# Kernel tuning notes

Measured on AMD Instinct MI355X. Metric: run time of the kernel, lower is better.

Reference implementation:

```python
import jax, jax.numpy as jnp
import numpy as np

H = 128
GATE_CODES = (2, 3, 4, 1)  # order in original forward: NOT, AND, OR, MAJ


def gru_step(x, h, Wih, bih, Whh, bhh):
    # single-step PyTorch GRU math; weights stored transposed [H, 3H]
    gi = x @ Wih + bih
    gh = h @ Whh + bhh
    ir, iz, inn = jnp.split(gi, 3, axis=-1)
    hr, hz, hn = jnp.split(gh, 3, axis=-1)
    r = jax.nn.sigmoid(ir + hr)
    z = jax.nn.sigmoid(iz + hz)
    n = jnp.tanh(inn + r * hn)
    return (1.0 - z) * n + z * h


def setup_inputs() -> dict:
    key = jax.random.key(0)
    N, E, L = 60000, 180000, 3
    ks = jax.random.split(key, 16)

    def p(k, shape, fan_in):
        return (jax.random.normal(k, shape, jnp.float32) / np.float32(np.sqrt(fan_in)))

    return dict(
        gate=jax.random.randint(ks[0], (N,), 0, 6),
        edge_index=jax.random.randint(ks[1], (2, E), 0, N),
        forward_level=jax.random.randint(ks[2], (N,), 0, L),
        num_levels=L,
        Ws_self=p(ks[3], (6, H), 6), Ws_nbr=p(ks[4], (6, H), 6),
        Wt_self=p(ks[5], (6, H), 6), Wt_nbr=p(ks[6], (6, H), 6),
        hs_W=p(ks[7], (2 * H, H), 2 * H), hs_b=jnp.zeros((H,), jnp.float32),
        aggr_W1=p(ks[8], (4, 2 * H, H), 2 * H), aggr_b1=jnp.zeros((4, H), jnp.float32),
        aggr_W2=p(ks[9], (4, H, H), H), aggr_b2=jnp.zeros((4, H), jnp.float32),
        gru_Wih=p(ks[10], (4, H, 3 * H), H), gru_bih=jnp.zeros((4, 3 * H), jnp.float32),
        gru_Whh=p(ks[11], (4, H, 3 * H), H), gru_bhh=jnp.zeros((4, 3 * H), jnp.float32),
    )


def reference(gate, edge_index, forward_level, num_levels,
              Ws_self, Ws_nbr, Wt_self, Wt_nbr, hs_W, hs_b,
              aggr_W1, aggr_b1, aggr_W2, aggr_b2,
              gru_Wih, gru_bih, gru_Whh, gru_bhh):
    N = gate.shape[0]
    src, dst = edge_index[0], edge_index[1]

    # struct encoder: one-hop MP producing source/target embeddings s, t [N, H]
    one_hot = jax.nn.one_hot(gate, 6, dtype=jnp.float32)
    nbr_in = jax.ops.segment_sum(one_hot[src], dst, num_segments=N)
    nbr_out = jax.ops.segment_sum(one_hot[dst], src, num_segments=N)
    s = jax.nn.relu(one_hot @ Ws_self + nbr_in @ Ws_nbr)
    t = jax.nn.relu(one_hot @ Wt_self + nbr_out @ Wt_nbr)

    hs = jnp.concatenate([s, t], -1) @ hs_W + hs_b          # [N, H]
    hf = jnp.zeros((N, H), jnp.float32)

    gate_dst = gate[dst]
    lvl_dst = forward_level[dst]
    # num_rounds = 1; levels 1..num_levels-1, gate types disjoint per node
    for level in range(1, num_levels):
        node_state = jnp.concatenate([hs, hf], -1)           # [N, 2H]
        src_state = node_state[src]                          # [E, 2H] gather
        for gi, code in enumerate(GATE_CODES):
            emask = ((gate_dst == code) & (lvl_dst == level)).astype(jnp.float32)[:, None]
            msg = jax.nn.relu(src_state @ aggr_W1[gi] + aggr_b1[gi]) @ aggr_W2[gi] + aggr_b2[gi]
            agg = jax.ops.segment_sum(msg * emask, dst, num_segments=N)  # scatter-add
            h_new = gru_step(agg, hf, gru_Wih[gi], gru_bih[gi], gru_Whh[gi], gru_bhh[gi])
            nmask = ((gate == code) & (forward_level == level))[:, None]
            hf = jnp.where(nmask, h_new, hf)
    return hs, hf
```

## Files before the change

### kernel.cpp

```cpp
#include <hip/hip_runtime.h>
#include <limits.h>

#define H 128

typedef __bf16 bf16x8 __attribute__((ext_vector_type(8)));
typedef __bf16 bf16x4 __attribute__((ext_vector_type(4)));
typedef float  f32x4  __attribute__((ext_vector_type(4)));

#define CUR_SENTINEL (INT_MIN / 2)

__device__ __forceinline__ int gate_to_gi(int g) {
    switch (g) {
        case 2: return 0;
        case 3: return 1;
        case 4: return 2;
        case 1: return 3;
        default: return -1;
    }
}

__global__ __launch_bounds__(256)
void prep_weights(const float* __restrict__ aW1, const float* __restrict__ aW2,
                  const float* __restrict__ gWih, const float* __restrict__ hsW,
                  __bf16* __restrict__ W1T, __bf16* __restrict__ W2T,
                  __bf16* __restrict__ WihT, __bf16* __restrict__ hsWT,
                  f32x4* __restrict__ zbase, int zn16) {
    const int z = blockIdx.z;
    const int tid = threadIdx.x;
    if (z == 14) {
        f32x4 zero = {};
        for (int i = blockIdx.x * 256 + tid; i < zn16; i += gridDim.x * 256) zbase[i] = zero;
        return;
    }
    const float* src;
    __bf16* dst;
    int K, C;
    if (z < 4)       { src = aW1 + (size_t)z * 256 * 128;       dst = W1T + (size_t)z * 128 * 256; K = 256; C = 128; }
    else if (z < 8)  { src = aW2 + (size_t)(z - 4) * 128 * 128; dst = W2T + (size_t)(z - 4) * 128 * 128; K = 128; C = 128; }
    else if (z < 12) { src = gWih + (size_t)(z - 8) * 128 * 384; dst = WihT + (size_t)(z - 8) * 384 * 128; K = 128; C = 384; }
    else             { src = hsW;                                dst = hsWT;                        K = 256; C = 128; }
    __shared__ float tile[32][33];
    const int tilesC = C >> 5;
    const int ntile = (K >> 5) * tilesC;
    const int t = blockIdx.x;
    if (t >= ntile) return;
    const int k0 = (t / tilesC) << 5;
    const int c0 = (t % tilesC) << 5;
    #pragma unroll
    for (int e = 0; e < 4; ++e) {
        int pos = e * 256 + tid;
        int kk = pos >> 5, cc = pos & 31;
        tile[kk][cc] = src[(size_t)(k0 + kk) * C + c0 + cc];
    }
    __syncthreads();
    #pragma unroll
    for (int e = 0; e < 4; ++e) {
        int pos = e * 256 + tid;
        int cc = pos >> 5, kk = pos & 31;
        dst[(size_t)(c0 + cc) * K + k0 + kk] = (__bf16)tile[kk][cc];
    }
}

__global__ __launch_bounds__(256)
void hist_kernel(const int* __restrict__ gate, const int* __restrict__ ei, int E,
                 int* __restrict__ cnt_in, int* __restrict__ cnt_out) {
    int e = blockIdx.x * blockDim.x + threadIdx.x;
    if (e >= E) return;
    int s = ei[e], d = ei[E + e];
    atomicAdd(&cnt_in[d * 6 + gate[s]], 1);
    atomicAdd(&cnt_out[s * 6 + gate[d]], 1);
}

__global__ __launch_bounds__(256)
void node_alloc(const int* __restrict__ gate, const int* __restrict__ lvl,
                const int* __restrict__ cnt_in, int N, int ecap, int ncap,
                int* __restrict__ galloc, int* __restrict__ ncnt,
                int* __restrict__ cursor, int* __restrict__ nbuf) {
    __shared__ int lcnt[16];
    __shared__ int lbase[16];
    const int tid = threadIdx.x;
    for (int base = blockIdx.x * 256; base < N; base += gridDim.x * 256) {
        if (tid < 16) lcnt[tid] = 0;
        __syncthreads();
        int n = base + tid;
        int b = -1, local = 0, nlocal = 0;
        if (n < N) {
            int gi = gate_to_gi(gate[n]);
            int L = lvl[n];
            if (gi >= 0 && L >= 1 && L <= 2) {
                b = (L - 1) * 4 + gi;
                int deg = 0;
                #pragma unroll
                for (int c = 0; c < 6; ++c) deg += cnt_in[n * 6 + c];
                local = atomicAdd(&lcnt[b], deg);
                nlocal = atomicAdd(&lcnt[8 + b], 1);
            }
        }
        __syncthreads();
        if (tid < 8)       lbase[tid] = atomicAdd(&galloc[tid], lcnt[tid]);
        else if (tid < 16) lbase[tid] = atomicAdd(&ncnt[tid - 8], lcnt[tid]);
        __syncthreads();
        if (n < N) {
            if (b >= 0) {
                cursor[n] = b * ecap + lbase[b] + local;
                int p = lbase[8 + b] + nlocal;
                if (p < ncap) nbuf[b * ncap + p] = n;
            } else {
                cursor[n] = CUR_SENTINEL;
            }
        }
        __syncthreads();
    }
}

__global__ __launch_bounds__(256)
void edge_scatter(const int* __restrict__ ei, int E,
                  int* __restrict__ cursor, int2* __restrict__ elist) {
    int e = blockIdx.x * blockDim.x + threadIdx.x;
    if (e >= E) return;
    int d = ei[E + e];
    int slot = atomicAdd(&cursor[d], 1);
    if (slot >= 0) elist[slot] = make_int2(ei[e], d);
}

__global__ __launch_bounds__(256, 2)
void encoder_mfma(const int* __restrict__ gate, const int* __restrict__ lvl,
                  const int* __restrict__ cnt_in, const int* __restrict__ cnt_out,
                  const float* __restrict__ Ws_self, const float* __restrict__ Ws_nbr,
                  const float* __restrict__ Wt_self, const float* __restrict__ Wt_nbr,
                  const __bf16* __restrict__ hsWT, const float* __restrict__ hs_b,
                  float* __restrict__ out, __bf16* __restrict__ mir,
                  float* __restrict__ agg, int N) {
    __shared__ __bf16 st[16][264];
    const int tid = threadIdx.x;
    const int lane = tid & 63;
    const int w = tid >> 6;
    const int row = tid >> 4;
    const int c0 = (tid & 15) * 8;

    bf16x8 bw[8][2];
    #pragma unroll
    for (int kk = 0; kk < 8; ++kk)
        #pragma unroll
        for (int j = 0; j < 2; ++j) {
            int col = w * 32 + j * 16 + (lane & 15);
            bw[kk][j] = *(const bf16x8*)&hsWT[(size_t)col * 256 + kk * 32 + (lane >> 4) * 8];
        }
    float hbc[2];
    #pragma unroll
    for (int j = 0; j < 2; ++j) hbc[j] = hs_b[w * 32 + j * 16 + (lane & 15)];

    const int ntiles = (N + 15) >> 4;
    for (int t = blockIdx.x; t < ntiles; t += gridDim.x) {
        const int base = t * 16;
        int n = base + row;
        if (n >= N) n = N - 1;
        const int g = gate[n];
        const int L = lvl[n];
        int cin[6], cout[6];
        #pragma unroll
        for (int k = 0; k < 6; ++k) { cin[k] = cnt_in[n * 6 + k]; cout[k] = cnt_out[n * 6 + k]; }
        f32x4 s0 = *(const f32x4*)&Ws_self[g * H + c0];
        f32x4 s1 = *(const f32x4*)&Ws_self[g * H + c0 + 4];
        f32x4 t0 = *(const f32x4*)&Wt_self[g * H + c0];
        f32x4 t1 = *(const f32x4*)&Wt_self[g * H + c0 + 4];
        #pragma unroll
        for (int k = 0; k < 6; ++k) {
            float ci = (float)cin[k], co = (float)cout[k];
            s0 += ci * *(const f32x4*)&Ws_nbr[k * H + c0];
            s1 += ci * *(const f32x4*)&Ws_nbr[k * H + c0 + 4];
            t0 += co * *(const f32x4*)&Wt_nbr[k * H + c0];
            t1 += co * *(const f32x4*)&Wt_nbr[k * H + c0 + 4];
        }
        bf16x8 ps, pt;
        #pragma unroll
        for (int j = 0; j < 4; ++j) {
            ps[j]     = (__bf16)fmaxf(s0[j], 0.f);
            ps[4 + j] = (__bf16)fmaxf(s1[j], 0.f);
            pt[j]     = (__bf16)fmaxf(t0[j], 0.f);
            pt[4 + j] = (__bf16)fmaxf(t1[j], 0.f);
        }
        *(bf16x8*)&st[row][c0]       = ps;
        *(bf16x8*)&st[row][128 + c0] = pt;
        if (base + row < N) {
            f32x4 z = {};
            bf16x8 zb = {};
            *(bf16x8*)&mir[(size_t)n * 256 + 128 + c0] = zb;
            const bool bucketed = (gate_to_gi(g) >= 0 && L >= 1 && L <= 2);
            if (bucketed) {
                *(f32x4*)&agg[(size_t)n * H + c0]     = z;
                *(f32x4*)&agg[(size_t)n * H + c0 + 4] = z;
            } else {
                *(f32x4*)&out[(size_t)N * H + (size_t)n * H + c0]     = z;
                *(f32x4*)&out[(size_t)N * H + (size_t)n * H + c0 + 4] = z;
            }
        }
        __syncthreads();
        f32x4 acc[2] = {};
        #pragma unroll
        for (int kk = 0; kk < 8; ++kk) {
            bf16x8 a = *(const bf16x8*)&st[lane & 15][kk * 32 + (lane >> 4) * 8];
            #pragma unroll
            for (int j = 0; j < 2; ++j)
                acc[j] = __builtin_amdgcn_mfma_f32_16x16x32_bf16(a, bw[kk][j], acc[j], 0, 0, 0);
        }
        #pragma unroll
        for (int j = 0; j < 2; ++j) {
            int col = w * 32 + j * 16 + (lane & 15);
            #pragma unroll
            for (int r = 0; r < 4; ++r) {
                int nn = base + (lane >> 4) * 4 + r;
                if (nn < N) {
                    float v = acc[j][r] + hbc[j];
                    out[(size_t)nn * H + col] = v;
                    mir[(size_t)nn * 256 + col] = (__bf16)v;
                }
            }
        }
        __syncthreads();
    }
}

template<int KHALF>
__global__ __launch_bounds__(256, 2)
void edge_msg_seg(int level, const int* __restrict__ etot,
                  const int2* __restrict__ elist, int ecap,
                  const __bf16* __restrict__ W1T, const __bf16* __restrict__ W2T,
                  const float* __restrict__ b1, const float* __restrict__ b2,
                  const __bf16* __restrict__ mir, float* __restrict__ agg) {
    const int gi = blockIdx.y;
    const int b = (level - 1) * 4 + gi;
    const int ecnt = etot[b];
    const int ntiles = (ecnt + 15) >> 4;
    if (ntiles == 0) return;

    __shared__ __bf16 st[16][264];
    __shared__ __bf16 hid[16][136];
    __shared__ float msgbuf[16][132];
    __shared__ int ssrc[16], sdst[16];
    __shared__ int leadrow[17];
    __shared__ int nlead;

    const int tid = threadIdx.x;
    const int lane = tid & 63;
    const int w = tid >> 6;
    const __bf16* w1 = W1T + (size_t)gi * 128 * 256;
    const __bf16* w2 = W2T + (size_t)gi * 128 * 128;

    bf16x8 w1f[KHALF][2], w2f[4][2];
    #pragma unroll
    for (int kk = 0; kk < KHALF; ++kk)
        #pragma unroll
        for (int j = 0; j < 2; ++j) {
            int col = w * 32 + j * 16 + (lane & 15);
            w1f[kk][j] = *(const bf16x8*)&w1[(size_t)col * 256 + kk * 32 + (lane >> 4) * 8];
        }
    #pragma unroll
    for (int kk = 0; kk < 4; ++kk)
        #pragma unroll
        for (int j = 0; j < 2; ++j) {
            int col = w * 32 + j * 16 + (lane & 15);
            w2f[kk][j] = *(const bf16x8*)&w2[(size_t)col * 128 + kk * 32 + (lane >> 4) * 8];
        }
    float b1c[2], b2c[2];
    #pragma unroll
    for (int j = 0; j < 2; ++j) {
        int col = w * 32 + j * 16 + (lane & 15);
        b1c[j] = b1[gi * H + col];
        b2c[j] = b2[gi * H + col];
    }

    for (int t = blockIdx.x; t < ntiles; t += gridDim.x) {
        const int base = t * 16;
        const int rem = min(16, ecnt - base);
        if (tid < 64) {
            if (tid < 16) {
                int2 e = elist[b * ecap + base + min(tid, rem - 1)];
                ssrc[tid] = e.x;
                sdst[tid] = e.y;
            }
            bool flag = (tid < rem) && (tid == 0 || sdst[tid] != sdst[tid - 1]);
            unsigned long long m = __ballot(flag);
            if (flag) {
                int rank = __popcll(m & ((1ull << tid) - 1));
                leadrow[rank] = tid;
            }
            if (tid == 0) {
                int nl = __popcll(m);
                nlead = nl;
                leadrow[nl] = rem;
            }
        }
        __syncthreads();
        #pragma unroll
        for (int rep = 0; rep < KHALF / 4; ++rep) {
            int idx = rep * 256 + tid;
            int r = idx / (KHALF * 4);
            int c = idx - r * (KHALF * 4);
            *(bf16x8*)&st[r][c * 8] = *(const bf16x8*)&mir[(size_t)ssrc[r] * 256 + c * 8];
        }
        __syncthreads();
        f32x4 acc[2] = {};
        #pragma unroll
        for (int kk = 0; kk < KHALF; ++kk) {
            bf16x8 a = *(const bf16x8*)&st[lane & 15][kk * 32 + (lane >> 4) * 8];
            #pragma unroll
            for (int j = 0; j < 2; ++j)
                acc[j] = __builtin_amdgcn_mfma_f32_16x16x32_bf16(a, w1f[kk][j], acc[j], 0, 0, 0);
        }
        #pragma unroll
        for (int j = 0; j < 2; ++j) {
            int col = w * 32 + j * 16 + (lane & 15);
            #pragma unroll
            for (int r = 0; r < 4; ++r)
                hid[(lane >> 4) * 4 + r][col] = (__bf16)fmaxf(acc[j][r] + b1c[j], 0.f);
        }
        __syncthreads();
        f32x4 acc2[2] = {};
        #pragma unroll
        for (int kk = 0; kk < 4; ++kk) {
            bf16x8 a = *(const bf16x8*)&hid[lane & 15][kk * 32 + (lane >> 4) * 8];
            #pragma unroll
            for (int j = 0; j < 2; ++j)
                acc2[j] = __builtin_amdgcn_mfma_f32_16x16x32_bf16(a, w2f[kk][j], acc2[j], 0, 0, 0);
        }
        #pragma unroll
        for (int j = 0; j < 2; ++j) {
            int col = w * 32 + j * 16 + (lane & 15);
            #pragma unroll
            for (int r = 0; r < 4; ++r)
                msgbuf[(lane >> 4) * 4 + r][col] = acc2[j][r] + b2c[j];
        }
        __syncthreads();
        const int nl = nlead;
        for (int idx = tid; idx < (nl << 7); idx += 256) {
            int li = idx >> 7, c = idx & 127;
            int r0 = leadrow[li], r1 = leadrow[li + 1];
            float s = msgbuf[r0][c];
            for (int r = r0 + 1; r < r1; ++r) s += msgbuf[r][c];
            atomicAdd(&agg[(size_t)sdst[r0] * H + c], s);
        }
        __syncthreads();
    }
}

__global__ __launch_bounds__(256, 2)
void gru_mfma(const int* __restrict__ ncnt, const int* __restrict__ nbuf, int ncap,
              int level, int N,
              const __bf16* __restrict__ WihT, const float* __restrict__ bih,
              const float* __restrict__ bhh,
              const float* __restrict__ agg, float* __restrict__ out,
              __bf16* __restrict__ mir) {
    const int gi = blockIdx.y;
    const int bucket = (level - 1) * 4 + gi;
    const int cnt = min(ncnt[bucket], ncap);
    const int ntiles = (cnt + 15) >> 4;
    if (ntiles == 0) return;

    __shared__ __bf16 x[16][136];
    __shared__ int nid[16];
    const int tid = threadIdx.x;
    const int lane = tid & 63;
    const int w = tid >> 6;
    const __bf16* wih = WihT + (size_t)gi * 384 * 128;

    bf16x8 wf[4][3][2];
    #pragma unroll
    for (int kk = 0; kk < 4; ++kk)
        #pragma unroll
        for (int p = 0; p < 3; ++p)
            #pragma unroll
            for (int j = 0; j < 2; ++j) {
                int oc = p * 128 + w * 32 + j * 16 + (lane & 15);
                wf[kk][p][j] = *(const bf16x8*)&wih[(size_t)oc * 128 + kk * 32 + (lane >> 4) * 8];
            }
    float bir[2], biz[2], bin[2], bhn[2];
    #pragma unroll
    for (int j = 0; j < 2; ++j) {
        int col = w * 32 + j * 16 + (lane & 15);
        bir[j] = bih[gi * 384 + col] + bhh[gi * 384 + col];
        biz[j] = bih[gi * 384 + 128 + col] + bhh[gi * 384 + 128 + col];
        bin[j] = bih[gi * 384 + 256 + col];
        bhn[j] = bhh[gi * 384 + 256 + col];
    }

    for (int t = blockIdx.x; t < ntiles; t += gridDim.x) {
        const int base = t * 16;
        const int rem = min(16, cnt - base);
        if (tid < 16) nid[tid] = nbuf[bucket * ncap + base + min(tid, rem - 1)];
        __syncthreads();
        #pragma unroll
        for (int rep = 0; rep < 2; ++rep) {
            int idx = rep * 256 + tid;
            int row = idx >> 5, c4 = idx & 31;
            f32x4 v = *(const f32x4*)&agg[(size_t)nid[row] * H + c4 * 4];
            bf16x4 p;
            p[0] = (__bf16)v[0]; p[1] = (__bf16)v[1]; p[2] = (__bf16)v[2]; p[3] = (__bf16)v[3];
            *(bf16x4*)&x[row][c4 * 4] = p;
        }
        __syncthreads();
        f32x4 acc[3][2] = {};
        #pragma unroll
        for (int kk = 0; kk < 4; ++kk) {
            bf16x8 a = *(const bf16x8*)&x[lane & 15][kk * 32 + (lane >> 4) * 8];
            #pragma unroll
            for (int p = 0; p < 3; ++p)
                #pragma unroll
                for (int j = 0; j < 2; ++j)
                    acc[p][j] = __builtin_amdgcn_mfma_f32_16x16x32_bf16(a, wf[kk][p][j], acc[p][j], 0, 0, 0);
        }
        #pragma unroll
        for (int j = 0; j < 2; ++j) {
            int col = w * 32 + j * 16 + (lane & 15);
            #pragma unroll
            for (int r = 0; r < 4; ++r) {
                int row = (lane >> 4) * 4 + r;
                if (row >= rem) continue;
                float rr = 1.f / (1.f + expf(-(acc[0][j][r] + bir[j])));
                float zz = 1.f / (1.f + expf(-(acc[1][j][r] + biz[j])));
                float nn = tanhf(acc[2][j][r] + bin[j] + rr * bhn[j]);
                float h = (1.f - zz) * nn;
                out[(size_t)N * H + (size_t)nid[row] * H + col] = h;
                mir[(size_t)nid[row] * 256 + 128 + col] = (__bf16)h;
            }
        }
        __syncthreads();
    }
}

extern "C" void kernel_launch(void* const* d_in, const int* in_sizes, int n_in,
                              void* d_out, int out_size, void* d_ws, size_t ws_size,
                              hipStream_t stream) {
    const int*   gate    = (const int*)d_in[0];
    const int*   ei      = (const int*)d_in[1];
    const int*   lvl     = (const int*)d_in[2];
    const float* Ws_self = (const float*)d_in[4];
    const float* Ws_nbr  = (const float*)d_in[5];
    const float* Wt_self = (const float*)d_in[6];
    const float* Wt_nbr  = (const float*)d_in[7];
    const float* hs_W    = (const float*)d_in[8];
    const float* hs_b    = (const float*)d_in[9];
    const float* aW1     = (const float*)d_in[10];
    const float* ab1     = (const float*)d_in[11];
    const float* aW2     = (const float*)d_in[12];
    const float* ab2     = (const float*)d_in[13];
    const float* gWih    = (const float*)d_in[14];
    const float* gbih    = (const float*)d_in[15];
    const float* gbhh    = (const float*)d_in[17];

    const int N = in_sizes[0];
    const int E = in_sizes[1] / 2;
    const int ECAP = ((E / 4) + 15) & ~15;
    const int NCAP = ((N / 4) + 15) & ~15;

    char* wsb = (char*)d_ws;
    size_t off = 0;
    float* agg = (float*)(wsb + off);         off += (size_t)N * H * sizeof(float);
    const size_t zstart = off;
    int* cnt_in = (int*)(wsb + off);          off += (size_t)N * 6 * sizeof(int);
    int* cnt_out = (int*)(wsb + off);         off += (size_t)N * 6 * sizeof(int);
    int* ncnt = (int*)(wsb + off);            off += 8 * sizeof(int);
    int* galloc = (int*)(wsb + off);          off += 8 * sizeof(int); off = (off + 63) & ~(size_t)63;
    const size_t zero_bytes = off - zstart;
    int* cursor = (int*)(wsb + off);          off += (size_t)N * sizeof(int); off = (off + 7) & ~(size_t)7;
    int2* elist = (int2*)(wsb + off);         off += (size_t)8 * ECAP * sizeof(int2);
    int* nbuf   = (int*)(wsb + off);          off += (size_t)8 * NCAP * sizeof(int);
    __bf16* mir = (__bf16*)(wsb + off);       off += (size_t)N * 256 * sizeof(__bf16);
    __bf16* W1T = (__bf16*)(wsb + off);       off += (size_t)4 * 128 * 256 * 2;
    __bf16* W2T = (__bf16*)(wsb + off);       off += (size_t)4 * 128 * 128 * 2;
    __bf16* WihT = (__bf16*)(wsb + off);      off += (size_t)4 * 384 * 128 * 2;
    __bf16* hsWT = (__bf16*)(wsb + off);      off += (size_t)128 * 256 * 2;

    float* out = (float*)d_out;

    prep_weights<<<dim3(48, 1, 15), 256, 0, stream>>>(
        aW1, aW2, gWih, hs_W, W1T, W2T, WihT, hsWT,
        (f32x4*)(wsb + zstart), (int)(zero_bytes / 16));
    hist_kernel<<<(E + 255) / 256, 256, 0, stream>>>(gate, ei, E, cnt_in, cnt_out);
    node_alloc<<<(N + 255) / 256, 256, 0, stream>>>(
        gate, lvl, cnt_in, N, ECAP, NCAP, galloc, ncnt, cursor, nbuf);
    edge_scatter<<<(E + 255) / 256, 256, 0, stream>>>(ei, E, cursor, elist);
    encoder_mfma<<<512, 256, 0, stream>>>(
        gate, lvl, cnt_in, cnt_out, Ws_self, Ws_nbr, Wt_self, Wt_nbr, hsWT, hs_b,
        out, mir, agg, N);

    edge_msg_seg<4><<<dim3(128, 4), 256, 0, stream>>>(
        1, galloc, elist, ECAP, W1T, W2T, ab1, ab2, mir, agg);
    gru_mfma<<<dim3(128, 4), 256, 0, stream>>>(
        ncnt, nbuf, NCAP, 1, N, WihT, gbih, gbhh, agg, out, mir);
    edge_msg_seg<8><<<dim3(128, 4), 256, 0, stream>>>(
        2, galloc, elist, ECAP, W1T, W2T, ab1, ab2, mir, agg);
    gru_mfma<<<dim3(128, 4), 256, 0, stream>>>(
        ncnt, nbuf, NCAP, 2, N, WihT, gbih, gbhh, agg, out, mir);
}
```

Measured before the change: 131.3 us.

## Fuse node allocation and encoder into one block-partitioned kernel launch

```diff
diff --git a/kernel.cpp b/kernel.cpp
--- a/kernel.cpp
+++ b/kernel.cpp
@@ -71,68 +71,60 @@
     atomicAdd(&cnt_out[s * 6 + gate[d]], 1);
 }
 
-__global__ __launch_bounds__(256)
-void node_alloc(const int* __restrict__ gate, const int* __restrict__ lvl,
-                const int* __restrict__ cnt_in, int N, int ecap, int ncap,
-                int* __restrict__ galloc, int* __restrict__ ncnt,
-                int* __restrict__ cursor, int* __restrict__ nbuf) {
-    __shared__ int lcnt[16];
-    __shared__ int lbase[16];
+__global__ __launch_bounds__(256, 2)
+void alloc_enc(const int* __restrict__ gate, const int* __restrict__ lvl,
+               const int* __restrict__ cnt_in, const int* __restrict__ cnt_out,
+               int N, int ECAP, int NCAP,
+               int* __restrict__ galloc, int* __restrict__ ncnt,
+               int* __restrict__ cursor, int* __restrict__ nbuf,
+               const float* __restrict__ Ws_self, const float* __restrict__ Ws_nbr,
+               const float* __restrict__ Wt_self, const float* __restrict__ Wt_nbr,
+               const __bf16* __restrict__ hsWT, const float* __restrict__ hs_b,
+               float* __restrict__ out, __bf16* __restrict__ mir,
+               float* __restrict__ agg, int AB) {
+    struct SA { int lcnt[16]; int lbase[16]; };
+    struct SE { __bf16 st[16][264]; };
+    __shared__ union { SA a; SE e; } sm;
     const int tid = threadIdx.x;
-    for (int base = blockIdx.x * 256; base < N; base += gridDim.x * 256) {
-        if (tid < 16) lcnt[tid] = 0;
-        __syncthreads();
-        int n = base + tid;
-        int b = -1, local = 0, nlocal = 0;
-        if (n < N) {
-            int gi = gate_to_gi(gate[n]);
-            int L = lvl[n];
-            if (gi >= 0 && L >= 1 && L <= 2) {
-                b = (L - 1) * 4 + gi;
-                int deg = 0;
-                #pragma unroll
-                for (int c = 0; c < 6; ++c) deg += cnt_in[n * 6 + c];
-                local = atomicAdd(&lcnt[b], deg);
-                nlocal = atomicAdd(&lcnt[8 + b], 1);
-            }
-        }
-        __syncthreads();
-        if (tid < 8)       lbase[tid] = atomicAdd(&galloc[tid], lcnt[tid]);
-        else if (tid < 16) lbase[tid] = atomicAdd(&ncnt[tid - 8], lcnt[tid]);
-        __syncthreads();
-        if (n < N) {
-            if (b >= 0) {
-                cursor[n] = b * ecap + lbase[b] + local;
-                int p = lbase[8 + b] + nlocal;
-                if (p < ncap) nbuf[b * ncap + p] = n;
-            } else {
-                cursor[n] = CUR_SENTINEL;
-            }
-        }
-        __syncthreads();
-    }
-}
-
-__global__ __launch_bounds__(256)
-void edge_scatter(const int* __restrict__ ei, int E,
-                  int* __restrict__ cursor, int2* __restrict__ elist) {
-    int e = blockIdx.x * blockDim.x + threadIdx.x;
-    if (e >= E) return;
-    int d = ei[E + e];
-    int slot = atomicAdd(&cursor[d], 1);
-    if (slot >= 0) elist[slot] = make_int2(ei[e], d);
-}
-
-__global__ __launch_bounds__(256, 2)
-void encoder_mfma(const int* __restrict__ gate, const int* __restrict__ lvl,
-                  const int* __restrict__ cnt_in, const int* __restrict__ cnt_out,
-                  const float* __restrict__ Ws_self, const float* __restrict__ Ws_nbr,
-                  const float* __restrict__ Wt_self, const float* __restrict__ Wt_nbr,
-                  const __bf16* __restrict__ hsWT, const float* __restrict__ hs_b,
-                  float* __restrict__ out, __bf16* __restrict__ mir,
-                  float* __restrict__ agg, int N) {
-    __shared__ __bf16 st[16][264];
-    const int tid = threadIdx.x;
+
+    if ((int)blockIdx.x < AB) {
+        for (int base = blockIdx.x * 256; base < N; base += AB * 256) {
+            if (tid < 16) sm.a.lcnt[tid] = 0;
+            __syncthreads();
+            int n = base + tid;
+            int b = -1, local = 0, nlocal = 0;
+            if (n < N) {
+                int gi = gate_to_gi(gate[n]);
+                int L = lvl[n];
+                if (gi >= 0 && L >= 1 && L <= 2) {
+                    b = (L - 1) * 4 + gi;
+                    int deg = 0;
+                    #pragma unroll
+                    for (int c = 0; c < 6; ++c) deg += cnt_in[n * 6 + c];
+                    local = atomicAdd(&sm.a.lcnt[b], deg);
+                    nlocal = atomicAdd(&sm.a.lcnt[8 + b], 1);
+                }
+            }
+            __syncthreads();
+            if (tid < 8)       sm.a.lbase[tid] = atomicAdd(&galloc[tid], sm.a.lcnt[tid]);
+            else if (tid < 16) sm.a.lbase[tid] = atomicAdd(&ncnt[tid - 8], sm.a.lcnt[tid]);
+            __syncthreads();
+            if (n < N) {
+                if (b >= 0) {
+                    cursor[n] = b * ECAP + sm.a.lbase[b] + local;
+                    int q = sm.a.lbase[8 + b] + nlocal;
+                    if (q < NCAP) nbuf[b * NCAP + q] = n;
+                } else {
+                    cursor[n] = CUR_SENTINEL;
+                }
+            }
+            __syncthreads();
+        }
+        return;
+    }
+
+    const int xb = blockIdx.x - AB;
+    const int xstep = gridDim.x - AB;
     const int lane = tid & 63;
     const int w = tid >> 6;
     const int row = tid >> 4;
@@ -151,7 +143,7 @@
     for (int j = 0; j < 2; ++j) hbc[j] = hs_b[w * 32 + j * 16 + (lane & 15)];
 
     const int ntiles = (N + 15) >> 4;
-    for (int t = blockIdx.x; t < ntiles; t += gridDim.x) {
+    for (int t = xb; t < ntiles; t += xstep) {
         const int base = t * 16;
         int n = base + row;
         if (n >= N) n = N - 1;
@@ -180,8 +172,8 @@
             pt[j]     = (__bf16)fmaxf(t0[j], 0.f);
             pt[4 + j] = (__bf16)fmaxf(t1[j], 0.f);
         }
-        *(bf16x8*)&st[row][c0]       = ps;
-        *(bf16x8*)&st[row][128 + c0] = pt;
+        *(bf16x8*)&sm.e.st[row][c0]       = ps;
+        *(bf16x8*)&sm.e.st[row][128 + c0] = pt;
         if (base + row < N) {
             f32x4 z = {};
             bf16x8 zb = {};
@@ -199,7 +191,7 @@
         f32x4 acc[2] = {};
         #pragma unroll
         for (int kk = 0; kk < 8; ++kk) {
-            bf16x8 a = *(const bf16x8*)&st[lane & 15][kk * 32 + (lane >> 4) * 8];
+            bf16x8 a = *(const bf16x8*)&sm.e.st[lane & 15][kk * 32 + (lane >> 4) * 8];
             #pragma unroll
             for (int j = 0; j < 2; ++j)
                 acc[j] = __builtin_amdgcn_mfma_f32_16x16x32_bf16(a, bw[kk][j], acc[j], 0, 0, 0);
@@ -219,6 +211,16 @@
         }
         __syncthreads();
     }
+}
+
+__global__ __launch_bounds__(256)
+void edge_scatter(const int* __restrict__ ei, int E,
+                  int* __restrict__ cursor, int2* __restrict__ elist) {
+    int e = blockIdx.x * blockDim.x + threadIdx.x;
+    if (e >= E) return;
+    int d = ei[E + e];
+    int slot = atomicAdd(&cursor[d], 1);
+    if (slot >= 0) elist[slot] = make_int2(ei[e], d);
 }
 
 template<int KHALF>
@@ -477,12 +479,10 @@
         aW1, aW2, gWih, hs_W, W1T, W2T, WihT, hsWT,
         (f32x4*)(wsb + zstart), (int)(zero_bytes / 16));
     hist_kernel<<<(E + 255) / 256, 256, 0, stream>>>(gate, ei, E, cnt_in, cnt_out);
-    node_alloc<<<(N + 255) / 256, 256, 0, stream>>>(
-        gate, lvl, cnt_in, N, ECAP, NCAP, galloc, ncnt, cursor, nbuf);
+    alloc_enc<<<512, 256, 0, stream>>>(
+        gate, lvl, cnt_in, cnt_out, N, ECAP, NCAP, galloc, ncnt, cursor, nbuf,
+        Ws_self, Ws_nbr, Wt_self, Wt_nbr, hsWT, hs_b, out, mir, agg, 64);
     edge_scatter<<<(E + 255) / 256, 256, 0, stream>>>(ei, E, cursor, elist);
-    encoder_mfma<<<512, 256, 0, stream>>>(
-        gate, lvl, cnt_in, cnt_out, Ws_self, Ws_nbr, Wt_self, Wt_nbr, hsWT, hs_b,
-        out, mir, agg, N);
 
     edge_msg_seg<4><<<dim3(128, 4), 256, 0, stream>>>(
         1, galloc, elist, ECAP, W1T, W2T, ab1, ab2, mir, agg);
```

New measurement: 129.9 us (median of 2 runs). About the same (-1.1%).
